# Kernel optimization log

Hardware: AMD Instinct MI355X
Metric: run time of the kernel (lower is better)

Reference implementation:

```python
import jax, jax.numpy as jnp
import numpy as np

B, T, P, D, H, L, C = 32, 50000, 100, 512, 16, 6, 256
SCALES = [1, 2, 4]
NS = len(SCALES)
HS = H // NS          # heads per scale = 5
KD = D // H           # key_dim = 32
N = T // P            # num_patches = 500
FF = 4 * D
EPS = 1e-3            # keras LayerNormalization default epsilon


def layernorm(x, g, b):
    m = jnp.mean(x, axis=-1, keepdims=True)
    v = jnp.var(x, axis=-1, keepdims=True)
    return (x - m) * jax.lax.rsqrt(v + EPS) * g + b


def mha(x, Wq, bq, Wk, bk, Wv, bv, Wo, bo):
    # keras MultiHeadAttention: self-attention, scale 1/sqrt(key_dim), biases on
    q = jnp.einsum('bnd,dhk->bnhk', x, Wq) + bq
    k = jnp.einsum('bnd,dhk->bnhk', x, Wk) + bk
    v = jnp.einsum('bnd,dhk->bnhk', x, Wv) + bv
    scores = jnp.einsum('bnhk,bmhk->bhnm', q, k) / jnp.sqrt(jnp.asarray(KD, x.dtype))
    p = jax.nn.softmax(scores, axis=-1)
    o = jnp.einsum('bhnm,bmhk->bnhk', p, v)
    return jnp.einsum('bnhk,hkd->bnd', o, Wo) + bo


def forward(inputs, ln_in_g, ln_in_b, patch_W, patch_b, pos_emb,
            Wq, bq, Wk, bk, Wv, bv, Wo, bo, Wc, bc,
            ln1_g, ln1_b, W1, b1, W2, b2, ln2_g, ln2_b, head_W, head_b):
    x = inputs[..., None]                       # (B, T, 1)
    x = layernorm(x, ln_in_g, ln_in_b)          # degenerate size-1 LN (faithful)
    patches = x.reshape(B, N, P)                # (B, N, P)
    h = patches @ patch_W + patch_b + pos_emb   # (B, N, D)
    for l in range(L):
        outs = []
        for si, s in enumerate(SCALES):
            if s > 1:
                pooled = h.reshape(B, N // s, s, D).mean(axis=2)  # SAME avg_pool1d (N % s == 0)
            else:
                pooled = h
            a = mha(pooled, Wq[l, si], bq[l, si], Wk[l, si], bk[l, si],
                    Wv[l, si], bv[l, si], Wo[l, si], bo[l, si])
            if s > 1:
                a = jnp.repeat(a, s, axis=1)[:, :N]
            outs.append(a)
        comb = jnp.concatenate(outs, axis=-1) @ Wc[l] + bc[l]
        h = h + comb
        h = layernorm(h, ln1_g[l], ln1_b[l])
        f = jax.nn.gelu(h @ W1[l] + b1[l], approximate=False)
        f = f @ W2[l] + b2[l]
        h = h + f
        h = layernorm(h, ln2_g[l], ln2_b[l])
        # Dropout(0.1) identity at inference
    g = h.mean(axis=1)                          # GlobalAveragePooling1D
    return jax.nn.softmax(g @ head_W + head_b, axis=-1)  # key head


def setup_inputs() -> dict:
    key = jax.random.key(0)
    ks = jax.random.split(key, 20)
    r = lambda k, sh, s=0.02: (jax.random.normal(k, sh, jnp.float32) * s)
    f32 = jnp.float32
    return {
        'inputs': jax.random.normal(ks[0], (B, T), f32),
        'ln_in_g': jnp.ones((1,), f32),
        'ln_in_b': r(ks[1], (1,)),
        'patch_W': r(ks[2], (P, D)),
        'patch_b': r(ks[3], (D,)),
        'pos_emb': r(ks[4], (1, N, D)),
        'Wq': r(ks[5], (L, NS, D, HS, KD)), 'bq': jnp.zeros((L, NS, HS, KD), f32),
        'Wk': r(ks[6], (L, NS, D, HS, KD)), 'bk': jnp.zeros((L, NS, HS, KD), f32),
        'Wv': r(ks[7], (L, NS, D, HS, KD)), 'bv': jnp.zeros((L, NS, HS, KD), f32),
        'Wo': r(ks[8], (L, NS, HS, KD, D)), 'bo': jnp.zeros((L, NS, D), f32),
        'Wc': r(ks[9], (L, NS * D, D)), 'bc': jnp.zeros((L, D), f32),
        'ln1_g': jnp.ones((L, D), f32), 'ln1_b': jnp.zeros((L, D), f32),
        'W1': r(ks[10], (L, D, FF)), 'b1': jnp.zeros((L, FF), f32),
        'W2': r(ks[11], (L, FF, D)), 'b2': jnp.zeros((L, D), f32),
        'ln2_g': jnp.ones((L, D), f32), 'ln2_b': jnp.zeros((L, D), f32),
        'head_W': r(ks[12], (D, C)), 'head_b': jnp.zeros((C,), f32),
    }


def reference(inputs, ln_in_g, ln_in_b, patch_W, patch_b, pos_emb,
              Wq, bq, Wk, bk, Wv, bv, Wo, bo, Wc, bc,
              ln1_g, ln1_b, W1, b1, W2, b2, ln2_g, ln2_b, head_W, head_b):
    return forward(inputs, ln_in_g, ln_in_b, patch_W, patch_b, pos_emb,
                   Wq, bq, Wk, bk, Wv, bv, Wo, bo, Wc, bc,
                   ln1_g, ln1_b, W1, b1, W2, b2, ln2_g, ln2_b, head_W, head_b)
```

## Files before the change

kernel.cpp:

```cpp
#include <hip/hip_runtime.h>
#include <math.h>


#define DD 512
#define NN 500
#define HSC 5
#define KDD 32
#define QKVN 160
#define QKV3 480
#define FF 2048
#define NL 6
#define NC 256
#define NB 32
#define LNEPS 1e-3f
#define BM 128
#define BN 64
#define KCHB 64

#define RTOT 875
#define OSZ 140000
#define MLSZ 4384
#define QSP 420000
#define W2CL 98304

typedef __attribute__((ext_vector_type(8))) short bf16x8;
typedef __attribute__((ext_vector_type(4))) float f32x4;

__device__ __forceinline__ float gelu_exact(float x) {
    return 0.5f * x * (1.0f + erff(x * 0.70710678118654752f));
}

__device__ __forceinline__ unsigned int pkbf(float a, float b) {
    unsigned int r;
    asm("v_cvt_pk_bf16_f32 %0, %1, %2" : "=v"(r) : "v"(a), "v"(b));
    return r;
}


template<int POOL, int TAIL>
__device__ __forceinline__ void mstage(
        const float* __restrict__ A, int lda,
        const float* __restrict__ Bcol, int ldb,
        int M, int bm, int k0, int klim,
        int ar4, int akq, int bkq,
        float4 (&aR)[2][4], float4 (&bR)[4]) {
    #pragma unroll
    for (int p = 0; p < 2; ++p) {
        int row = min(bm + ar4 + p * 64, M - 1);
        const float* ap = A + (size_t)row * POOL * lda;
        #pragma unroll
        for (int i = 0; i < 4; ++i) {
            int kk = akq + i * 4;
            int kg = TAIL ? min(k0 + kk, klim - 4) : (k0 + kk);
            float4 v = *(const float4*)(ap + kg);
            #pragma unroll
            for (int t = 1; t < POOL; ++t) {
                float4 u = *(const float4*)(ap + kg + (size_t)t * lda);
                v.x += u.x; v.y += u.y; v.z += u.z; v.w += u.w;
            }
            if (POOL > 1) {
                const float ip = 1.0f / (float)POOL;
                v.x *= ip; v.y *= ip; v.z *= ip; v.w *= ip;
            }
            if (TAIL) {
                bool ok = (k0 + kk) < klim;
                v.x = ok ? v.x : 0.f; v.y = ok ? v.y : 0.f;
                v.z = ok ? v.z : 0.f; v.w = ok ? v.w : 0.f;
            }
            aR[p][i] = v;
        }
    }
    #pragma unroll
    for (int i = 0; i < 4; ++i) {
        int kr = TAIL ? min(k0 + bkq + i, klim - 1) : (k0 + bkq + i);
        bR[i] = *(const float4*)(Bcol + (size_t)kr * ldb);
    }
}

#define CHUNK_LDS_WRITE() { \
    _Pragma("unroll") \
    for (int p = 0; p < 2; ++p) { \
        int r = ar4 + p * 64; \
        int swz = (r & 7) << 4; \
        char* base = (char*)As + r * 128; \
        _Pragma("unroll") \
        for (int i = 0; i < 4; ++i) { \
            int cb = (akq + i * 4) * 2; \
            *(uint2*)(base + (cb ^ swz)) = make_uint2( \
                pkbf(aR[p][i].x, aR[p][i].y), pkbf(aR[p][i].z, aR[p][i].w)); \
        } \
    } \
    { \
        const float* b0 = (const float*)&bR[0]; \
        const float* b1 = (const float*)&bR[1]; \
        const float* b2 = (const float*)&bR[2]; \
        const float* b3 = (const float*)&bR[3]; \
        _Pragma("unroll") \
        for (int j = 0; j < 4; ++j) { \
            int nrow = bn4 * 4 + j; \
            char* base = (char*)Bs + nrow * 128; \
            *(uint2*)(base + ((bkq * 2) ^ ((nrow & 7) << 4))) = make_uint2( \
                pkbf(b0[j], b1[j]), pkbf(b2[j], b3[j])); \
        } \
    } }

#define CHUNK_MFMA() { \
    _Pragma("unroll") \
    for (int half = 0; half < 2; ++half) { \
        const int kb = (half * 32 + (lane >> 4) * 8) * 2; \
        bf16x8 af[4], bf[2]; \
        _Pragma("unroll") \
        for (int m = 0; m < 4; ++m) { \
            int r = wm * 64 + m * 16 + (lane & 15); \
            af[m] = *(const bf16x8*)((const char*)As + r * 128 + (kb ^ ((r & 7) << 4))); \
        } \
        _Pragma("unroll") \
        for (int n = 0; n < 2; ++n) { \
            int r = wn * 32 + n * 16 + (lane & 15); \
            bf[n] = *(const bf16x8*)((const char*)Bs + r * 128 + (kb ^ ((r & 7) << 4))); \
        } \
        _Pragma("unroll") \
        for (int m = 0; m < 4; ++m) \
            _Pragma("unroll") \
            for (int n = 0; n < 2; ++n) \
                acc[m][n] = __builtin_amdgcn_mfma_f32_16x16x32_bf16( \
                    af[m], bf[n], acc[m][n], 0, 0, 0); \
    } }

template<int POOL, int TAIL>
__device__ __forceinline__ void mfma_core(
        const float* __restrict__ A, int lda,
        const float* __restrict__ Bcol, int ldb,
        int M, int bm, int ks, int nch, int klim, f32x4 (&acc)[4][2]) {
    __shared__ __align__(16) unsigned short As[128 * 64];
    __shared__ __align__(16) unsigned short Bs[64 * 64];
    const int tid = threadIdx.x;
    const int ar4 = tid >> 2, akq = (tid & 3) * 16;
    const int bkq = (tid >> 4) * 4, bn4 = tid & 15;
    const int lane = tid & 63, wid = tid >> 6;
    const int wm = wid >> 1, wn = wid & 1;

    float4 aR[2][4], bR[4];
    mstage<POOL, TAIL>(A, lda, Bcol, ldb, M, bm, ks, klim,
                       ar4, akq, bkq, aR, bR);

    for (int c = 0; c < nch; ++c) {
        __syncthreads();
        CHUNK_LDS_WRITE();
        __syncthreads();
        if (c + 1 < nch)
            mstage<POOL, TAIL>(A, lda, Bcol, ldb, M, bm,
                               ks + (c + 1) * KCHB, klim,
                               ar4, akq, bkq, aR, bR);
        CHUNK_MFMA();
    }
}

#define MACC_INIT(acc) { _Pragma("unroll") for (int m_ = 0; m_ < 4; ++m_) \
    _Pragma("unroll") for (int n_ = 0; n_ < 2; ++n_) \
    _Pragma("unroll") for (int j_ = 0; j_ < 4; ++j_) acc[m_][n_][j_] = 0.f; }

__global__ void colsum_kernel(const float* __restrict__ pw, float* __restrict__ csum) {
    int d = blockIdx.x * blockDim.x + threadIdx.x;
    if (d < DD) {
        float s = 0.f;
        for (int p = 0; p < 100; ++p) s += pw[p * DD + d];
        csum[d] = s;
    }
}

__global__ void init_h(const float* __restrict__ csum, const float* __restrict__ pb,
                       const float* __restrict__ pos, const float* __restrict__ lnb,
                       float* __restrict__ h) {
    int idx = blockIdx.x * 256 + threadIdx.x;
    if (idx >= NN * DD) return;
    int d = idx & (DD - 1);
    h[idx] = lnb[0] * csum[d] + pb[d] + pos[idx];
}

__global__ __launch_bounds__(256, 2) void w2c_pre(
        const float* __restrict__ Wo, const float* __restrict__ Wc,
        float* __restrict__ w2c) {
    int z = blockIdx.z;
    int l = z / 3, s = z - l * 3;
    int bm = blockIdx.y * BM, bn = blockIdx.x * BN;
    int tid = threadIdx.x;
    const float* A = Wo + (size_t)z * QKVN * DD;
    const float* Bcol = Wc + (size_t)l * 1536 * DD + (size_t)s * DD * DD
                      + bn + (tid & 15) * 4;
    f32x4 acc[4][2];
    MACC_INIT(acc);
    mfma_core<1, 0>(A, DD, Bcol, DD, QKVN, bm, 0, 8, DD, acc);

    float* C = w2c + (size_t)z * W2CL;
    int lane = tid & 63, wid = tid >> 6, wm = wid >> 1, wn = wid & 1;
    #pragma unroll
    for (int q = 0; q < 2; ++q) {
        int c2 = bn + wn * 32 + q * 16 + (lane & 15);
        #pragma unroll
        for (int m = 0; m < 4; ++m) {
            int r0 = bm + wm * 64 + m * 16 + ((lane >> 4) << 2);
            #pragma unroll
            for (int j = 0; j < 4; ++j) {
                int r = r0 + j;
                if (r < QKVN) C[(size_t)r * DD + c2] = acc[m][q][j];
                else if (r < 192) C[(size_t)r * DD + c2] = 0.f;
            }
        }
    }
}

__global__ void bconst_part(const float* __restrict__ bo,
                            const float* __restrict__ Wc,
                            float* __restrict__ bpart) {
    int z = blockIdx.x, ch = blockIdx.y;
    int l = z / 3, s = z - l * 3;
    int t = threadIdx.x;
    int j0 = ch * 64;
    const float* bp = bo + (size_t)z * DD + j0;
    const float* wp = Wc + (size_t)l * 1536 * DD + (size_t)s * DD * DD
                    + (size_t)j0 * DD;
    float a0 = 0.f, a1 = 0.f;
    for (int j = 0; j < 64; ++j) {
        float b = bp[j];
        a0 += b * wp[(size_t)j * DD + t];
        a1 += b * wp[(size_t)j * DD + t + 256];
    }
    float* op = bpart + ((size_t)z * 8 + ch) * DD;
    op[t] = a0;
    op[t + 256] = a1;
}

__global__ void bconst_fin(const float* __restrict__ bpart,
                           const float* __restrict__ bc,
                           float* __restrict__ bconst) {
    int l = blockIdx.x, d = threadIdx.x;
    float acc = bc[(size_t)l * DD + d];
    const float* bp = bpart + (size_t)l * 3 * 8 * DD;
    #pragma unroll
    for (int i = 0; i < 24; ++i) acc += bp[(size_t)i * DD + d];
    bconst[(size_t)l * DD + d] = acc;
}

__global__ __launch_bounds__(256, 2) void qkv_part(
        const float* __restrict__ h,
        const float* __restrict__ Wq, const float* __restrict__ Wk,
        const float* __restrict__ Wv,
        float* __restrict__ part, int l) {
    int scale = blockIdx.z >> 2, ps = blockIdx.z & 3;
    int n = NN >> scale;
    int bm = blockIdx.y * BM;
    if (bm >= n) return;
    int bn = blockIdx.x * BN;
    size_t w = (size_t)(l * 3 + scale);
    int tid = threadIdx.x;
    int col = min(bn + (tid & 15) * 4, QKV3 - 4);
    int which = (col >= 320) ? 2 : ((col >= 160) ? 1 : 0);
    const float* Wsel = (which == 0) ? Wq : ((which == 1) ? Wk : Wv);
    const float* Bcol = Wsel + w * DD * QKVN + (col - which * QKVN);
    float* outb = part + (size_t)ps * QSP
                + (scale == 0 ? 0 : (scale == 1 ? 240000 : 360000));

    f32x4 acc[4][2];
    MACC_INIT(acc);
    if (scale == 0)
        mfma_core<1, 0>(h, DD, Bcol, QKVN, n, bm, ps * 128, 2, DD, acc);
    else if (scale == 1)
        mfma_core<2, 0>(h, DD, Bcol, QKVN, n, bm, ps * 128, 2, DD, acc);
    else
        mfma_core<4, 0>(h, DD, Bcol, QKVN, n, bm, ps * 128, 2, DD, acc);

    int lane = tid & 63, wid = tid >> 6, wm = wid >> 1, wn = wid & 1;
    #pragma unroll
    for (int q = 0; q < 2; ++q) {
        int cb = bn + wn * 32 + q * 16;
        if (cb >= QKV3) continue;
        int c2 = cb + (lane & 15);
        #pragma unroll
        for (int m = 0; m < 4; ++m) {
            int r0 = bm + wm * 64 + m * 16 + ((lane >> 4) << 2);
            #pragma unroll
            for (int j = 0; j < 4; ++j) {
                int r = r0 + j;
                if (r < n) outb[(size_t)r * QKV3 + c2] = acc[m][q][j];
            }
        }
    }
}

__global__ void qkv_reduce(const float* __restrict__ part,
                           const float* __restrict__ bq,
                           const float* __restrict__ bk,
                           const float* __restrict__ bv,
                           float* __restrict__ qkvAll, int l) {
    int idx = blockIdx.x * 256 + threadIdx.x;
    if (idx >= 420000) return;
    int scale, base;
    if (idx < 240000) { scale = 0; base = 0; }
    else if (idx < 360000) { scale = 1; base = 240000; }
    else { scale = 2; base = 360000; }
    int rowrem = (idx - base) % QKV3;
    int which = rowrem / QKVN;
    int col = rowrem - which * QKVN;
    float v = part[idx] + part[QSP + idx]
            + part[2 * QSP + idx] + part[3 * QSP + idx];
    v += ((which == 0) ? bq : (which == 1 ? bk : bv))[(size_t)(l * 3 + scale) * QKVN + col];
    qkvAll[idx] = v;
}

__global__ __launch_bounds__(256, 2) void attn_split(
        const float* __restrict__ qkvAll, float* __restrict__ oPart,
        float* __restrict__ mPart, float* __restrict__ lPart) {
    int z = blockIdx.z;
    int scale, sp;
    if (z < 8)       { scale = 0; sp = z; }
    else if (z < 12) { scale = 1; sp = z - 8; }
    else             { scale = 2; sp = z - 12; }
    int n = NN >> scale;
    int qt = blockIdx.x;
    if (qt * 64 >= n) return;
    int hh = blockIdx.y;
    int ks = sp * 64;
    int ke = min(n, ks + 64);
    const float* qkv = qkvAll + (scale == 0 ? 0 : (scale == 1 ? 240000 : 360000));
    int rowb = (scale == 0 ? 0 : (scale == 1 ? 500 : 750));

    int tid = threadIdx.x;
    int kg = tid & 7, qq = tid >> 3;
    int q0 = qt * 64 + qq, q1 = q0 + 32;
    bool ok0 = q0 < n, ok1 = q1 < n;

    float qa[32], qb[32];
    {
        const float* p0 = qkv + (size_t)(ok0 ? q0 : 0) * QKV3 + hh * KDD;
        const float* p1 = qkv + (size_t)(ok1 ? q1 : 0) * QKV3 + hh * KDD;
        #pragma unroll
        for (int c4 = 0; c4 < 8; ++c4) {
            float4 v0 = *(const float4*)(p0 + c4 * 4);
            float4 v1 = *(const float4*)(p1 + c4 * 4);
            qa[c4 * 4] = v0.x; qa[c4 * 4 + 1] = v0.y; qa[c4 * 4 + 2] = v0.z; qa[c4 * 4 + 3] = v0.w;
            qb[c4 * 4] = v1.x; qb[c4 * 4 + 1] = v1.y; qb[c4 * 4 + 2] = v1.z; qb[c4 * 4 + 3] = v1.w;
        }
    }

    __shared__ float Ks[64][36];
    __shared__ float Vs[64][36];
    float o0[32], o1[32];
    #pragma unroll
    for (int c = 0; c < 32; ++c) { o0[c] = 0.f; o1[c] = 0.f; }
    float m0 = -1e30f, m1 = -1e30f, l0 = 0.f, l1 = 0.f;

    int srow = tid >> 2, scol = tid & 3;

    {
        int kc = ks;
        int krow = kc + srow;
        bool ok = krow < ke;
        const float* kp = qkv + (size_t)(ok ? krow : 0) * QKV3 + QKVN + hh * KDD;
        #pragma unroll
        for (int half = 0; half < 2; ++half) {
            int cc = (half * 4 + scol) * 4;
            float4 kv = ok ? *(const float4*)(kp + cc) : make_float4(0.f, 0.f, 0.f, 0.f);
            float4 vv = ok ? *(const float4*)(kp + QKVN + cc) : make_float4(0.f, 0.f, 0.f, 0.f);
            Ks[srow][cc] = kv.x; Ks[srow][cc + 1] = kv.y; Ks[srow][cc + 2] = kv.z; Ks[srow][cc + 3] = kv.w;
            Vs[srow][cc] = vv.x; Vs[srow][cc + 1] = vv.y; Vs[srow][cc + 2] = vv.z; Vs[srow][cc + 3] = vv.w;
        }
        __syncthreads();

        float p0[8], p1[8];
        float cm = -1e30f;
        #pragma unroll
        for (int jj = 0; jj < 8; ++jj) {
            int j = jj * 8 + kg;
            float s0 = 0.f, s1 = 0.f;
            #pragma unroll
            for (int c4 = 0; c4 < 8; ++c4) {
                float4 kv = *(const float4*)&Ks[j][c4 * 4];
                s0 += qa[c4 * 4] * kv.x + qa[c4 * 4 + 1] * kv.y
                    + qa[c4 * 4 + 2] * kv.z + qa[c4 * 4 + 3] * kv.w;
                s1 += qb[c4 * 4] * kv.x + qb[c4 * 4 + 1] * kv.y
                    + qb[c4 * 4 + 2] * kv.z + qb[c4 * 4 + 3] * kv.w;
            }
            s0 *= 0.17677669529663687f;
            s1 *= 0.17677669529663687f;
            if (kc + j >= ke) { s0 = -1e30f; s1 = -1e30f; }
            p0[jj] = s0; p1[jj] = s1;
            cm = fmaxf(cm, fmaxf(s0, s1));
        }
        cm = fmaxf(cm, __shfl_xor(cm, 1));
        cm = fmaxf(cm, __shfl_xor(cm, 2));
        cm = fmaxf(cm, __shfl_xor(cm, 4));

        m0 = cm; m1 = cm;
        #pragma unroll
        for (int jj = 0; jj < 8; ++jj) {
            p0[jj] = expf(p0[jj] - cm); l0 += p0[jj];
            p1[jj] = expf(p1[jj] - cm); l1 += p1[jj];
        }
        #pragma unroll
        for (int jj = 0; jj < 8; ++jj) {
            int j = jj * 8 + kg;
            float w0 = p0[jj], w1 = p1[jj];
            #pragma unroll
            for (int c4 = 0; c4 < 8; ++c4) {
                float4 vv = *(const float4*)&Vs[j][c4 * 4];
                o0[c4 * 4]     += w0 * vv.x; o0[c4 * 4 + 1] += w0 * vv.y;
                o0[c4 * 4 + 2] += w0 * vv.z; o0[c4 * 4 + 3] += w0 * vv.w;
                o1[c4 * 4]     += w1 * vv.x; o1[c4 * 4 + 1] += w1 * vv.y;
                o1[c4 * 4 + 2] += w1 * vv.z; o1[c4 * 4 + 3] += w1 * vv.w;
            }
        }
    }
    #pragma unroll
    for (int st = 1; st < 8; st <<= 1) {
        l0 += __shfl_xor(l0, st);
        l1 += __shfl_xor(l1, st);
        #pragma unroll
        for (int c = 0; c < 32; ++c) {
            o0[c] += __shfl_xor(o0[c], st);
            o1[c] += __shfl_xor(o1[c], st);
        }
    }
    if (kg == 0) {
        float* ob = oPart + (size_t)sp * OSZ;
        if (ok0) {
            int r = rowb + q0;
            float* op = ob + (size_t)r * QKVN + hh * KDD;
            #pragma unroll
            for (int c4 = 0; c4 < 8; ++c4) {
                float4 v; v.x = o0[c4*4]; v.y = o0[c4*4+1]; v.z = o0[c4*4+2]; v.w = o0[c4*4+3];
                *(float4*)(op + c4 * 4) = v;
            }
            mPart[sp * MLSZ + r * HSC + hh] = m0;
            lPart[sp * MLSZ + r * HSC + hh] = l0;
        }
        if (ok1) {
            int r = rowb + q1;
            float* op = ob + (size_t)r * QKVN + hh * KDD;
            #pragma unroll
            for (int c4 = 0; c4 < 8; ++c4) {
                float4 v; v.x = o1[c4*4]; v.y = o1[c4*4+1]; v.z = o1[c4*4+2]; v.w = o1[c4*4+3];
                *(float4*)(op + c4 * 4) = v;
            }
            mPart[sp * MLSZ + r * HSC + hh] = m1;
            lPart[sp * MLSZ + r * HSC + hh] = l1;
        }
    }
}

__global__ void attn_combine(const float* __restrict__ oPart,
                             const float* __restrict__ mPart,
                             const float* __restrict__ lPart,
                             float* __restrict__ oAll) {
    int idx = blockIdx.x * 256 + threadIdx.x;
    if (idx >= OSZ) return;
    int rh = idx >> 5;
    int r = rh / HSC, hh = rh - r * HSC;
    int scale = (r < 500) ? 0 : (r < 750 ? 1 : 2);
    int ns = 8 >> scale;
    float M = -1e30f;
    for (int s = 0; s < ns; ++s) M = fmaxf(M, mPart[s * MLSZ + r * HSC + hh]);
    float L = 0.f, val = 0.f;
    for (int s = 0; s < ns; ++s) {
        float wgt = expf(mPart[s * MLSZ + r * HSC + hh] - M);
        L += wgt * lPart[s * MLSZ + r * HSC + hh];
        val += wgt * oPart[(size_t)s * OSZ + idx];
    }
    oAll[idx] = val / L;
}

__global__ __launch_bounds__(256, 2) void comb_gather(
        const float* __restrict__ oAll, const float* __restrict__ w2c,
        float* __restrict__ part, int l) {
    int sp = blockIdx.z;
    int si = (sp >= 6) ? 2 : (sp >= 3 ? 1 : 0);
    int kseg = (sp - si * 3) << 6;
    int bm = blockIdx.y * BM, bn = blockIdx.x * BN;
    int tid = threadIdx.x;
    const int soff = (si == 0) ? 0 : (si == 1 ? 80000 : 120000);
    const float* Bcol = w2c + (size_t)(l * 3 + si) * W2CL
                      + (size_t)kseg * DD + bn + (tid & 15) * 4;

    __shared__ __align__(16) unsigned short As[128 * 64];
    __shared__ __align__(16) unsigned short Bs[64 * 64];
    const int ar4 = tid >> 2, akq = (tid & 3) * 16;
    const int bkq = (tid >> 4) * 4, bn4 = tid & 15;
    const int lane = tid & 63, wid = tid >> 6;
    const int wm = wid >> 1, wn = wid & 1;

    f32x4 acc[4][2];
    MACC_INIT(acc);
    float4 aR[2][4], bR[4];

    #pragma unroll
    for (int p = 0; p < 2; ++p) {
        int row = min(bm + ar4 + p * 64, NN - 1);
        const float* ap = oAll + soff + (size_t)(row >> si) * QKVN;
        #pragma unroll
        for (int i = 0; i < 4; ++i) {
            int kk = kseg + akq + i * 4;
            int kg2 = min(kk, QKVN - 4);
            aR[p][i] = *(const float4*)(ap + kg2);
        }
    }
    #pragma unroll
    for (int i = 0; i < 4; ++i)
        bR[i] = *(const float4*)(Bcol + (size_t)(bkq + i) * DD);

    __syncthreads();
    CHUNK_LDS_WRITE();
    __syncthreads();
    CHUNK_MFMA();

    float* pz = part + (size_t)sp * NN * DD;
    #pragma unroll
    for (int q = 0; q < 2; ++q) {
        int c2 = bn + wn * 32 + q * 16 + (lane & 15);
        #pragma unroll
        for (int m = 0; m < 4; ++m) {
            int r0 = bm + wm * 64 + m * 16 + ((lane >> 4) << 2);
            #pragma unroll
            for (int j = 0; j < 4; ++j) {
                int r = r0 + j;
                if (r < NN) pz[(size_t)r * DD + c2] = acc[m][q][j];
            }
        }
    }
}

__global__ __launch_bounds__(256, 2) void w1_part(
        const float* __restrict__ h, const float* __restrict__ W1,
        float* __restrict__ part) {
    int sp = blockIdx.z;
    int bm = blockIdx.y * BM, bn = blockIdx.x * BN;
    int tid = threadIdx.x;
    const float* Bcol = W1 + bn + (tid & 15) * 4;
    f32x4 acc[4][2];
    MACC_INIT(acc);
    mfma_core<1, 0>(h, DD, Bcol, FF, NN, bm, sp * 128, 2, DD, acc);

    float* pz = part + (size_t)sp * NN * FF;
    int lane = tid & 63, wid = tid >> 6, wm = wid >> 1, wn = wid & 1;
    #pragma unroll
    for (int q = 0; q < 2; ++q) {
        int c2 = bn + wn * 32 + q * 16 + (lane & 15);
        #pragma unroll
        for (int m = 0; m < 4; ++m) {
            int r0 = bm + wm * 64 + m * 16 + ((lane >> 4) << 2);
            #pragma unroll
            for (int j = 0; j < 4; ++j) {
                int r = r0 + j;
                if (r < NN) pz[(size_t)r * FF + c2] = acc[m][q][j];
            }
        }
    }
}

__global__ void w1_reduce(const float* __restrict__ part,
                          const float* __restrict__ b1, float* __restrict__ f) {
    int idx = blockIdx.x * 256 + threadIdx.x;
    if (idx >= NN * FF) return;
    float v = part[idx] + part[NN * FF + idx]
            + part[2 * NN * FF + idx] + part[3 * NN * FF + idx];
    f[idx] = gelu_exact(v + b1[idx & (FF - 1)]);
}

__global__ __launch_bounds__(256, 2) void w2_part(
        const float* __restrict__ f, const float* __restrict__ W2,
        float* __restrict__ part) {
    int sp = blockIdx.z;
    int bm = blockIdx.y * BM, bn = blockIdx.x * BN;
    int tid = threadIdx.x;
    const float* Bcol = W2 + bn + (tid & 15) * 4;
    f32x4 acc[4][2];
    MACC_INIT(acc);
    mfma_core<1, 0>(f, FF, Bcol, DD, NN, bm, sp * 128, 2, FF, acc);

    float* pz = part + (size_t)sp * NN * DD;
    int lane = tid & 63, wid = tid >> 6, wm = wid >> 1, wn = wid & 1;
    #pragma unroll
    for (int q = 0; q < 2; ++q) {
        int c2 = bn + wn * 32 + q * 16 + (lane & 15);
        #pragma unroll
        for (int m = 0; m < 4; ++m) {
            int r0 = bm + wm * 64 + m * 16 + ((lane >> 4) << 2);
            #pragma unroll
            for (int j = 0; j < 4; ++j) {
                int r = r0 + j;
                if (r < NN) pz[(size_t)r * DD + c2] = acc[m][q][j];
            }
        }
    }
}

__global__ void reduce_add_ln(const float* __restrict__ part, int S,
                              const float* __restrict__ bias,
                              float* __restrict__ h,
                              const float* __restrict__ gw,
                              const float* __restrict__ bw) {
    int row = blockIdx.x, t = threadIdx.x;
    size_t idx = (size_t)row * DD + t;
    float x = h[idx] + bias[t];
    for (int s = 0; s < S; ++s) x += part[(size_t)s * NN * DD + idx];
    int lane = t & 63, wv = t >> 6;
    __shared__ float s1[8], s2[8];
    __shared__ float mb[2];
    float sum = x, sq = x * x;
    for (int off = 32; off; off >>= 1) {
        sum += __shfl_down(sum, off);
        sq  += __shfl_down(sq,  off);
    }
    if (lane == 0) { s1[wv] = sum; s2[wv] = sq; }
    __syncthreads();
    if (t == 0) {
        float a = 0.f, b = 0.f;
        for (int i = 0; i < 8; ++i) { a += s1[i]; b += s2[i]; }
        float mean = a / (float)DD;
        float var = b / (float)DD - mean * mean;
        mb[0] = mean;
        mb[1] = rsqrtf(var + LNEPS);
    }
    __syncthreads();
    h[idx] = (x - mb[0]) * mb[1] * gw[t] + bw[t];
}

__global__ void col_mean_part(const float* __restrict__ h, float* __restrict__ partial) {
    int col = blockIdx.x * 256 + threadIdx.x;
    int r0 = blockIdx.y * 20;
    float s = 0.f;
    #pragma unroll
    for (int r = 0; r < 20; ++r) s += h[(size_t)(r0 + r) * DD + col];
    partial[(size_t)blockIdx.y * DD + col] = s;
}

__global__ void head_kernel(const float* __restrict__ partial,
                            const float* __restrict__ hw,
                            const float* __restrict__ hb, float* __restrict__ out) {
    __shared__ float gs[DD];
    __shared__ float r[4];
    __shared__ float bmx, bsum;
    int t = threadIdx.x;
    for (int d = t; d < DD; d += 256) {
        float s = 0.f;
        #pragma unroll
        for (int p = 0; p < 25; ++p) s += partial[(size_t)p * DD + d];
        gs[d] = s / (float)NN;
    }
    __syncthreads();
    float acc = hb[t];
    #pragma unroll 16
    for (int d = 0; d < DD; ++d) acc += gs[d] * hw[(size_t)d * NC + t];
    int lane = t & 63, wv = t >> 6;
    float mx = acc;
    for (int off = 32; off; off >>= 1) mx = fmaxf(mx, __shfl_down(mx, off));
    if (lane == 0) r[wv] = mx;
    __syncthreads();
    if (t == 0) bmx = fmaxf(fmaxf(r[0], r[1]), fmaxf(r[2], r[3]));
    __syncthreads();
    float e = expf(acc - bmx);
    float s = e;
    for (int off = 32; off; off >>= 1) s += __shfl_down(s, off);
    if (lane == 0) r[wv] = s;
    __syncthreads();
    if (t == 0) bsum = 1.f / (r[0] + r[1] + r[2] + r[3]);
    __syncthreads();
    float pv = e * bsum;
    for (int b = 0; b < NB; ++b) out[(size_t)b * NC + t] = pv;
}

extern "C" void kernel_launch(void* const* d_in, const int* in_sizes, int n_in,
                              void* d_out, int out_size, void* d_ws, size_t ws_size,
                              hipStream_t stream) {
    const float* ln_in_b = (const float*)d_in[2];
    const float* patch_W = (const float*)d_in[3];
    const float* patch_b = (const float*)d_in[4];
    const float* pos_emb = (const float*)d_in[5];
    const float* Wq = (const float*)d_in[6];
    const float* bq = (const float*)d_in[7];
    const float* Wk = (const float*)d_in[8];
    const float* bk = (const float*)d_in[9];
    const float* Wv = (const float*)d_in[10];
    const float* bv = (const float*)d_in[11];
    const float* Wo = (const float*)d_in[12];
    const float* bo = (const float*)d_in[13];
    const float* Wc = (const float*)d_in[14];
    const float* bc = (const float*)d_in[15];
    const float* ln1_g = (const float*)d_in[16];
    const float* ln1_b = (const float*)d_in[17];
    const float* W1 = (const float*)d_in[18];
    const float* b1 = (const float*)d_in[19];
    const float* W2 = (const float*)d_in[20];
    const float* b2 = (const float*)d_in[21];
    const float* ln2_g = (const float*)d_in[22];
    const float* ln2_b = (const float*)d_in[23];
    const float* head_W = (const float*)d_in[24];
    const float* head_b = (const float*)d_in[25];
    float* out = (float*)d_out;

    float* ws = (float*)d_ws;
    float* h      = ws;
    float* csum   = h + 256000;
    float* qkvAll = csum + 1024;
    float* oAll   = qkvAll + 420000;
    float* f      = oAll + 140000;
    float* part   = f + 1024000;
    float* headp  = part + 4194304;
    float* w2c    = headp + 12800;
    float* bconst = w2c + 1769472;
    float* bpart  = bconst + 3072;
    float* qkvP   = part;
    float* oPart  = part + 1680000;
    float* mPart  = oPart + 1120000;
    float* lPart  = mPart + 8 * MLSZ;

    colsum_kernel<<<1, 512, 0, stream>>>(patch_W, csum);
    init_h<<<(NN * DD + 255) / 256, 256, 0, stream>>>(csum, patch_b, pos_emb, ln_in_b, h);
    w2c_pre<<<dim3(8, 2, 18), 256, 0, stream>>>(Wo, Wc, w2c);
    bconst_part<<<dim3(18, 8), 256, 0, stream>>>(bo, Wc, bpart);
    bconst_fin<<<NL, DD, 0, stream>>>(bpart, bc, bconst);

    for (int l = 0; l < NL; ++l) {
        qkv_part<<<dim3(8, 4, 12), 256, 0, stream>>>(h, Wq, Wk, Wv, qkvP, l);
        qkv_reduce<<<(420000 + 255) / 256, 256, 0, stream>>>(qkvP, bq, bk, bv, qkvAll, l);
        attn_split<<<dim3(8, HSC, 14), 256, 0, stream>>>(qkvAll, oPart, mPart, lPart);
        attn_combine<<<(OSZ + 255) / 256, 256, 0, stream>>>(oPart, mPart, lPart, oAll);
        comb_gather<<<dim3(8, 4, 9), 256, 0, stream>>>(oAll, w2c, part, l);
        reduce_add_ln<<<NN, DD, 0, stream>>>(part, 9, bconst + (size_t)l * DD, h,
                                             ln1_g + (size_t)l * DD, ln1_b + (size_t)l * DD);
        w1_part<<<dim3(32, 4, 4), 256, 0, stream>>>(
            h, W1 + (size_t)l * DD * FF, part);
        w1_reduce<<<(NN * FF + 255) / 256, 256, 0, stream>>>(
            part, b1 + (size_t)l * FF, f);
        w2_part<<<dim3(8, 4, 16), 256, 0, stream>>>(f, W2 + (size_t)l * FF * DD, part);
        reduce_add_ln<<<NN, DD, 0, stream>>>(part, 16, b2 + (size_t)l * DD, h,
                                             ln2_g + (size_t)l * DD, ln2_b + (size_t)l * DD);
    }
    col_mean_part<<<dim3(2, 25), 256, 0, stream>>>(h, headp);
    head_kernel<<<1, 256, 0, stream>>>(headp, head_W, head_b, out);
}
```

Measured before the change: 743.7 us.

## Drop split-K for QKV and W1 GEMMs, fuse bias/GELU epilogues, use 128-wide K chunks

Replaces the 64-wide K-chunk MFMA core with a 128-wide variant that doubles LDS tiles and staging registers. The QKV and W1 GEMMs now run full K per block and apply bias (and GELU for W1) in the epilogue. This removes the separate partial-sum reduce kernels and their global round-trips. W2 split-K drops from 16 to 8 partitions. The trade-off is far fewer blocks for the QKV and W1 GEMMs (96 and 128) and higher LDS and register use per block, which may reduce occupancy and parallelism on a GPU with many CUs.

```diff
diff --git a/kernel.cpp b/kernel.cpp
--- a/kernel.cpp
+++ b/kernel.cpp
@@ -15,12 +15,10 @@
 #define LNEPS 1e-3f
 #define BM 128
 #define BN 64
-#define KCHB 64
 
 #define RTOT 875
 #define OSZ 140000
 #define MLSZ 4384
-#define QSP 420000
 #define W2CL 98304
 
 typedef __attribute__((ext_vector_type(8))) short bf16x8;
@@ -37,45 +35,131 @@
 }
 
 
-template<int POOL, int TAIL>
-__device__ __forceinline__ void mstage(
+template<int POOL>
+__device__ __forceinline__ void mstage128(
         const float* __restrict__ A, int lda,
         const float* __restrict__ Bcol, int ldb,
-        int M, int bm, int k0, int klim,
-        int ar4, int akq, int bkq,
-        float4 (&aR)[2][4], float4 (&bR)[4]) {
+        int M, int bm, int k0,
+        int ar, int akq, int bkq,
+        float4 (&aR)[2][8], float4 (&bR)[8]) {
     #pragma unroll
     for (int p = 0; p < 2; ++p) {
-        int row = min(bm + ar4 + p * 64, M - 1);
-        const float* ap = A + (size_t)row * POOL * lda;
-        #pragma unroll
-        for (int i = 0; i < 4; ++i) {
-            int kk = akq + i * 4;
-            int kg = TAIL ? min(k0 + kk, klim - 4) : (k0 + kk);
-            float4 v = *(const float4*)(ap + kg);
-            #pragma unroll
-            for (int t = 1; t < POOL; ++t) {
-                float4 u = *(const float4*)(ap + kg + (size_t)t * lda);
-                v.x += u.x; v.y += u.y; v.z += u.z; v.w += u.w;
-            }
-            if (POOL > 1) {
-                const float ip = 1.0f / (float)POOL;
-                v.x *= ip; v.y *= ip; v.z *= ip; v.w *= ip;
-            }
-            if (TAIL) {
-                bool ok = (k0 + kk) < klim;
-                v.x = ok ? v.x : 0.f; v.y = ok ? v.y : 0.f;
-                v.z = ok ? v.z : 0.f; v.w = ok ? v.w : 0.f;
-            }
-            aR[p][i] = v;
-        }
-    }
-    #pragma unroll
-    for (int i = 0; i < 4; ++i) {
-        int kr = TAIL ? min(k0 + bkq + i, klim - 1) : (k0 + bkq + i);
-        bR[i] = *(const float4*)(Bcol + (size_t)kr * ldb);
-    }
-}
+        int row = min(bm + ar + p * 64, M - 1);
+        const float* ap = A + (size_t)row * POOL * lda + k0;
+        #pragma unroll
+        for (int hf = 0; hf < 2; ++hf) {
+            #pragma unroll
+            for (int i = 0; i < 4; ++i) {
+                int kk = hf * 64 + akq + i * 4;
+                float4 v = *(const float4*)(ap + kk);
+                #pragma unroll
+                for (int t = 1; t < POOL; ++t) {
+                    float4 u = *(const float4*)(ap + kk + (size_t)t * lda);
+                    v.x += u.x; v.y += u.y; v.z += u.z; v.w += u.w;
+                }
+                if (POOL > 1) {
+                    const float ip = 1.0f / (float)POOL;
+                    v.x *= ip; v.y *= ip; v.z *= ip; v.w *= ip;
+                }
+                aR[p][hf * 4 + i] = v;
+            }
+        }
+    }
+    #pragma unroll
+    for (int hf = 0; hf < 2; ++hf)
+        #pragma unroll
+        for (int i = 0; i < 4; ++i)
+            bR[hf * 4 + i] = *(const float4*)(Bcol
+                + (size_t)(k0 + hf * 64 + bkq + i) * ldb);
+}
+
+#define CHUNK128_LDS_WRITE() { \
+    _Pragma("unroll") \
+    for (int p = 0; p < 2; ++p) { \
+        int r = ar + p * 64; \
+        int swz = (r & 7) << 4; \
+        char* base = (char*)As + r * 256; \
+        _Pragma("unroll") \
+        for (int hf = 0; hf < 2; ++hf) { \
+            _Pragma("unroll") \
+            for (int i = 0; i < 4; ++i) { \
+                int cb = (hf * 64 + akq + i * 4) * 2; \
+                float4 v = aR[p][hf * 4 + i]; \
+                *(uint2*)(base + (cb ^ swz)) = make_uint2( \
+                    pkbf(v.x, v.y), pkbf(v.z, v.w)); \
+            } \
+        } \
+    } \
+    _Pragma("unroll") \
+    for (int j = 0; j < 4; ++j) { \
+        int nrow = bn4 * 4 + j; \
+        int swz = (nrow & 7) << 4; \
+        char* base = (char*)Bs + nrow * 256; \
+        _Pragma("unroll") \
+        for (int hf = 0; hf < 2; ++hf) { \
+            const float* q0 = (const float*)&bR[hf * 4 + 0]; \
+            const float* q1 = (const float*)&bR[hf * 4 + 1]; \
+            const float* q2 = (const float*)&bR[hf * 4 + 2]; \
+            const float* q3 = (const float*)&bR[hf * 4 + 3]; \
+            int cb = (hf * 64 + bkq) * 2; \
+            *(uint2*)(base + (cb ^ swz)) = make_uint2( \
+                pkbf(q0[j], q1[j]), pkbf(q2[j], q3[j])); \
+        } \
+    } }
+
+#define CHUNK128_MFMA() { \
+    _Pragma("unroll") \
+    for (int hf = 0; hf < 4; ++hf) { \
+        const int kb = (hf * 32 + (lane >> 4) * 8) * 2; \
+        bf16x8 af[4], bf[2]; \
+        _Pragma("unroll") \
+        for (int m = 0; m < 4; ++m) { \
+            int r = wm * 64 + m * 16 + (lane & 15); \
+            af[m] = *(const bf16x8*)((const char*)As + r * 256 + (kb ^ ((r & 7) << 4))); \
+        } \
+        _Pragma("unroll") \
+        for (int n = 0; n < 2; ++n) { \
+            int r = wn * 32 + n * 16 + (lane & 15); \
+            bf[n] = *(const bf16x8*)((const char*)Bs + r * 256 + (kb ^ ((r & 7) << 4))); \
+        } \
+        _Pragma("unroll") \
+        for (int m = 0; m < 4; ++m) \
+            _Pragma("unroll") \
+            for (int n = 0; n < 2; ++n) \
+                acc[m][n] = __builtin_amdgcn_mfma_f32_16x16x32_bf16( \
+                    af[m], bf[n], acc[m][n], 0, 0, 0); \
+    } }
+
+template<int POOL>
+__device__ __forceinline__ void mfma_core128(
+        const float* __restrict__ A, int lda,
+        const float* __restrict__ Bcol, int ldb,
+        int M, int bm, int ks, int nch, f32x4 (&acc)[4][2]) {
+    __shared__ __align__(16) unsigned short As[128 * 128];
+    __shared__ __align__(16) unsigned short Bs[64 * 128];
+    const int tid = threadIdx.x;
+    const int ar = tid >> 2, akq = (tid & 3) * 16;
+    const int bkq = (tid >> 4) * 4, bn4 = tid & 15;
+    const int lane = tid & 63, wid = tid >> 6;
+    const int wm = wid >> 1, wn = wid & 1;
+
+    float4 aR[2][8], bR[8];
+    mstage128<POOL>(A, lda, Bcol, ldb, M, bm, ks, ar, akq, bkq, aR, bR);
+
+    for (int c = 0; c < nch; ++c) {
+        __syncthreads();
+        CHUNK128_LDS_WRITE();
+        __syncthreads();
+        if (c + 1 < nch)
+            mstage128<POOL>(A, lda, Bcol, ldb, M, bm, ks + (c + 1) * 128,
+                            ar, akq, bkq, aR, bR);
+        CHUNK128_MFMA();
+    }
+}
+
+#define MACC_INIT(acc) { _Pragma("unroll") for (int m_ = 0; m_ < 4; ++m_) \
+    _Pragma("unroll") for (int n_ = 0; n_ < 2; ++n_) \
+    _Pragma("unroll") for (int j_ = 0; j_ < 4; ++j_) acc[m_][n_][j_] = 0.f; }
 
 #define CHUNK_LDS_WRITE() { \
     _Pragma("unroll") \
@@ -106,8 +190,8 @@
 
 #define CHUNK_MFMA() { \
     _Pragma("unroll") \
-    for (int half = 0; half < 2; ++half) { \
-        const int kb = (half * 32 + (lane >> 4) * 8) * 2; \
+    for (int hf = 0; hf < 2; ++hf) { \
+        const int kb = (hf * 32 + (lane >> 4) * 8) * 2; \
         bf16x8 af[4], bf[2]; \
         _Pragma("unroll") \
         for (int m = 0; m < 4; ++m) { \
@@ -126,39 +210,6 @@
                 acc[m][n] = __builtin_amdgcn_mfma_f32_16x16x32_bf16( \
                     af[m], bf[n], acc[m][n], 0, 0, 0); \
     } }
-
-template<int POOL, int TAIL>
-__device__ __forceinline__ void mfma_core(
-        const float* __restrict__ A, int lda,
-        const float* __restrict__ Bcol, int ldb,
-        int M, int bm, int ks, int nch, int klim, f32x4 (&acc)[4][2]) {
-    __shared__ __align__(16) unsigned short As[128 * 64];
-    __shared__ __align__(16) unsigned short Bs[64 * 64];
-    const int tid = threadIdx.x;
-    const int ar4 = tid >> 2, akq = (tid & 3) * 16;
-    const int bkq = (tid >> 4) * 4, bn4 = tid & 15;
-    const int lane = tid & 63, wid = tid >> 6;
-    const int wm = wid >> 1, wn = wid & 1;
-
-    float4 aR[2][4], bR[4];
-    mstage<POOL, TAIL>(A, lda, Bcol, ldb, M, bm, ks, klim,
-                       ar4, akq, bkq, aR, bR);
-
-    for (int c = 0; c < nch; ++c) {
-        __syncthreads();
-        CHUNK_LDS_WRITE();
-        __syncthreads();
-        if (c + 1 < nch)
-            mstage<POOL, TAIL>(A, lda, Bcol, ldb, M, bm,
-                               ks + (c + 1) * KCHB, klim,
-                               ar4, akq, bkq, aR, bR);
-        CHUNK_MFMA();
-    }
-}
-
-#define MACC_INIT(acc) { _Pragma("unroll") for (int m_ = 0; m_ < 4; ++m_) \
-    _Pragma("unroll") for (int n_ = 0; n_ < 2; ++n_) \
-    _Pragma("unroll") for (int j_ = 0; j_ < 4; ++j_) acc[m_][n_][j_] = 0.f; }
 
 __global__ void colsum_kernel(const float* __restrict__ pw, float* __restrict__ csum) {
     int d = blockIdx.x * blockDim.x + threadIdx.x;
@@ -190,7 +241,7 @@
                       + bn + (tid & 15) * 4;
     f32x4 acc[4][2];
     MACC_INIT(acc);
-    mfma_core<1, 0>(A, DD, Bcol, DD, QKVN, bm, 0, 8, DD, acc);
+    mfma_core128<1>(A, DD, Bcol, DD, QKVN, bm, 0, 4, acc);
 
     float* C = w2c + (size_t)z * W2CL;
     int lane = tid & 63, wid = tid >> 6, wm = wid >> 1, wn = wid & 1;
@@ -242,12 +293,14 @@
     bconst[(size_t)l * DD + d] = acc;
 }
 
-__global__ __launch_bounds__(256, 2) void qkv_part(
+__global__ __launch_bounds__(256, 2) void qkv_fused(
         const float* __restrict__ h,
         const float* __restrict__ Wq, const float* __restrict__ Wk,
         const float* __restrict__ Wv,
-        float* __restrict__ part, int l) {
-    int scale = blockIdx.z >> 2, ps = blockIdx.z & 3;
+        const float* __restrict__ bq, const float* __restrict__ bk,
+        const float* __restrict__ bv,
+        float* __restrict__ qkvAll, int l) {
+    int scale = blockIdx.z;
     int n = NN >> scale;
     int bm = blockIdx.y * BM;
     if (bm >= n) return;
@@ -258,54 +311,36 @@
     int which = (col >= 320) ? 2 : ((col >= 160) ? 1 : 0);
     const float* Wsel = (which == 0) ? Wq : ((which == 1) ? Wk : Wv);
     const float* Bcol = Wsel + w * DD * QKVN + (col - which * QKVN);
-    float* outb = part + (size_t)ps * QSP
-                + (scale == 0 ? 0 : (scale == 1 ? 240000 : 360000));
+    float* outb = qkvAll + (scale == 0 ? 0 : (scale == 1 ? 240000 : 360000));
 
     f32x4 acc[4][2];
     MACC_INIT(acc);
     if (scale == 0)
-        mfma_core<1, 0>(h, DD, Bcol, QKVN, n, bm, ps * 128, 2, DD, acc);
+        mfma_core128<1>(h, DD, Bcol, QKVN, n, bm, 0, 4, acc);
     else if (scale == 1)
-        mfma_core<2, 0>(h, DD, Bcol, QKVN, n, bm, ps * 128, 2, DD, acc);
+        mfma_core128<2>(h, DD, Bcol, QKVN, n, bm, 0, 4, acc);
     else
-        mfma_core<4, 0>(h, DD, Bcol, QKVN, n, bm, ps * 128, 2, DD, acc);
+        mfma_core128<4>(h, DD, Bcol, QKVN, n, bm, 0, 4, acc);
 
     int lane = tid & 63, wid = tid >> 6, wm = wid >> 1, wn = wid & 1;
     #pragma unroll
     for (int q = 0; q < 2; ++q) {
         int cb = bn + wn * 32 + q * 16;
         if (cb >= QKV3) continue;
+        int wq = (cb >= 320) ? 2 : ((cb >= 160) ? 1 : 0);
+        const float* bp = (wq == 0) ? bq : ((wq == 1) ? bk : bv);
         int c2 = cb + (lane & 15);
+        float bias = bp[w * QKVN + (cb - wq * QKVN) + (lane & 15)];
         #pragma unroll
         for (int m = 0; m < 4; ++m) {
             int r0 = bm + wm * 64 + m * 16 + ((lane >> 4) << 2);
             #pragma unroll
             for (int j = 0; j < 4; ++j) {
                 int r = r0 + j;
-                if (r < n) outb[(size_t)r * QKV3 + c2] = acc[m][q][j];
-            }
-        }
-    }
-}
-
-__global__ void qkv_reduce(const float* __restrict__ part,
-                           const float* __restrict__ bq,
-                           const float* __restrict__ bk,
-                           const float* __restrict__ bv,
-                           float* __restrict__ qkvAll, int l) {
-    int idx = blockIdx.x * 256 + threadIdx.x;
-    if (idx >= 420000) return;
-    int scale, base;
-    if (idx < 240000) { scale = 0; base = 0; }
-    else if (idx < 360000) { scale = 1; base = 240000; }
-    else { scale = 2; base = 360000; }
-    int rowrem = (idx - base) % QKV3;
-    int which = rowrem / QKVN;
-    int col = rowrem - which * QKVN;
-    float v = part[idx] + part[QSP + idx]
-            + part[2 * QSP + idx] + part[3 * QSP + idx];
-    v += ((which == 0) ? bq : (which == 1 ? bk : bv))[(size_t)(l * 3 + scale) * QKVN + col];
-    qkvAll[idx] = v;
+                if (r < n) outb[(size_t)r * QKV3 + c2] = acc[m][q][j] + bias;
+            }
+        }
+    }
 }
 
 __global__ __launch_bounds__(256, 2) void attn_split(
@@ -358,8 +393,8 @@
         bool ok = krow < ke;
         const float* kp = qkv + (size_t)(ok ? krow : 0) * QKV3 + QKVN + hh * KDD;
         #pragma unroll
-        for (int half = 0; half < 2; ++half) {
-            int cc = (half * 4 + scol) * 4;
+        for (int hf = 0; hf < 2; ++hf) {
+            int cc = (hf * 4 + scol) * 4;
             float4 kv = ok ? *(const float4*)(kp + cc) : make_float4(0.f, 0.f, 0.f, 0.f);
             float4 vv = ok ? *(const float4*)(kp + QKVN + cc) : make_float4(0.f, 0.f, 0.f, 0.f);
             Ks[srow][cc] = kv.x; Ks[srow][cc + 1] = kv.y; Ks[srow][cc + 2] = kv.z; Ks[srow][cc + 3] = kv.w;
@@ -528,41 +563,31 @@
     }
 }
 
-__global__ __launch_bounds__(256, 2) void w1_part(
+__global__ __launch_bounds__(256, 2) void w1_fused(
         const float* __restrict__ h, const float* __restrict__ W1,
-        float* __restrict__ part) {
-    int sp = blockIdx.z;
+        const float* __restrict__ b1, float* __restrict__ f) {
     int bm = blockIdx.y * BM, bn = blockIdx.x * BN;
     int tid = threadIdx.x;
     const float* Bcol = W1 + bn + (tid & 15) * 4;
     f32x4 acc[4][2];
     MACC_INIT(acc);
-    mfma_core<1, 0>(h, DD, Bcol, FF, NN, bm, sp * 128, 2, DD, acc);
-
-    float* pz = part + (size_t)sp * NN * FF;
+    mfma_core128<1>(h, DD, Bcol, FF, NN, bm, 0, 4, acc);
+
     int lane = tid & 63, wid = tid >> 6, wm = wid >> 1, wn = wid & 1;
     #pragma unroll
     for (int q = 0; q < 2; ++q) {
         int c2 = bn + wn * 32 + q * 16 + (lane & 15);
+        float bv_ = b1[c2];
         #pragma unroll
         for (int m = 0; m < 4; ++m) {
             int r0 = bm + wm * 64 + m * 16 + ((lane >> 4) << 2);
             #pragma unroll
             for (int j = 0; j < 4; ++j) {
                 int r = r0 + j;
-                if (r < NN) pz[(size_t)r * FF + c2] = acc[m][q][j];
-            }
-        }
-    }
-}
-
-__global__ void w1_reduce(const float* __restrict__ part,
-                          const float* __restrict__ b1, float* __restrict__ f) {
-    int idx = blockIdx.x * 256 + threadIdx.x;
-    if (idx >= NN * FF) return;
-    float v = part[idx] + part[NN * FF + idx]
-            + part[2 * NN * FF + idx] + part[3 * NN * FF + idx];
-    f[idx] = gelu_exact(v + b1[idx & (FF - 1)]);
+                if (r < NN) f[(size_t)r * FF + c2] = gelu_exact(acc[m][q][j] + bv_);
+            }
+        }
+    }
 }
 
 __global__ __launch_bounds__(256, 2) void w2_part(
@@ -574,7 +599,7 @@
     const float* Bcol = W2 + bn + (tid & 15) * 4;
     f32x4 acc[4][2];
     MACC_INIT(acc);
-    mfma_core<1, 0>(f, FF, Bcol, DD, NN, bm, sp * 128, 2, FF, acc);
+    mfma_core128<1>(f, FF, Bcol, DD, NN, bm, sp * 256, 2, acc);
 
     float* pz = part + (size_t)sp * NN * DD;
     int lane = tid & 63, wid = tid >> 6, wm = wid >> 1, wn = wid & 1;
@@ -708,8 +733,7 @@
     float* w2c    = headp + 12800;
     float* bconst = w2c + 1769472;
     float* bpart  = bconst + 3072;
-    float* qkvP   = part;
-    float* oPart  = part + 1680000;
+    float* oPart  = part + 2304000;
     float* mPart  = oPart + 1120000;
     float* lPart  = mPart + 8 * MLSZ;
 
@@ -720,19 +744,17 @@
     bconst_fin<<<NL, DD, 0, stream>>>(bpart, bc, bconst);
 
     for (int l = 0; l < NL; ++l) {
-        qkv_part<<<dim3(8, 4, 12), 256, 0, stream>>>(h, Wq, Wk, Wv, qkvP, l);
-        qkv_reduce<<<(420000 + 255) / 256, 256, 0, stream>>>(qkvP, bq, bk, bv, qkvAll, l);
+        qkv_fused<<<dim3(8, 4, 3), 256, 0, stream>>>(h, Wq, Wk, Wv, bq, bk, bv,
+                                                     qkvAll, l);
         attn_split<<<dim3(8, HSC, 14), 256, 0, stream>>>(qkvAll, oPart, mPart, lPart);
         attn_combine<<<(OSZ + 255) / 256, 256, 0, stream>>>(oPart, mPart, lPart, oAll);
         comb_gather<<<dim3(8, 4, 9), 256, 0, stream>>>(oAll, w2c, part, l);
         reduce_add_ln<<<NN, DD, 0, stream>>>(part, 9, bconst + (size_t)l * DD, h,
                                              ln1_g + (size_t)l * DD, ln1_b + (size_t)l * DD);
-        w1_part<<<dim3(32, 4, 4), 256, 0, stream>>>(
-            h, W1 + (size_t)l * DD * FF, part);
-        w1_reduce<<<(NN * FF + 255) / 256, 256, 0, stream>>>(
-            part, b1 + (size_t)l * FF, f);
-        w2_part<<<dim3(8, 4, 16), 256, 0, stream>>>(f, W2 + (size_t)l * FF * DD, part);
-        reduce_add_ln<<<NN, DD, 0, stream>>>(part, 16, b2 + (size_t)l * DD, h,
+        w1_fused<<<dim3(32, 4), 256, 0, stream>>>(
+            h, W1 + (size_t)l * DD * FF, b1 + (size_t)l * FF, f);
+        w2_part<<<dim3(8, 4, 8), 256, 0, stream>>>(f, W2 + (size_t)l * FF * DD, part);
+        reduce_add_ln<<<NN, DD, 0, stream>>>(part, 8, b2 + (size_t)l * DD, h,
                                              ln2_g + (size_t)l * DD, ln2_b + (size_t)l * DD);
     }
     col_mean_part<<<dim3(2, 25), 256, 0, stream>>>(h, headp);
```

Result: slower. 808.1 us (+8.7%).
